# Kernel optimization log

Measured on AMD Instinct MI355X. Metric: run time of the kernel, lower is better.

## Reference

```python
import jax, jax.numpy as jnp
import numpy as np

S, B, D, H, V, TOK = 512, 32, 512, 512, 64, 30000
L = 2  # num LSTM layers


def _lstm_dir(x, Wih, Whh, bih, bhh, reverse):
    # x: [S, B, Din]; Wih: [4H, Din]; Whh: [4H, H]
    Bn = x.shape[1]
    Hn = Whh.shape[1]

    def step(carry, xt):
        h, c = carry
        g = xt @ Wih.T + h @ Whh.T + bih + bhh  # [B, 4H]
        i, f, gg, o = jnp.split(g, 4, axis=-1)  # torch gate order i,f,g,o
        c = jax.nn.sigmoid(f) * c + jax.nn.sigmoid(i) * jnp.tanh(gg)
        h = jax.nn.sigmoid(o) * jnp.tanh(c)
        return (h, c), h

    init = (jnp.zeros((Bn, Hn), x.dtype), jnp.zeros((Bn, Hn), x.dtype))
    _, hs = jax.lax.scan(step, init, x, reverse=reverse)
    return hs  # [S, B, H], time-aligned with x


def _bilstm(x, Wih0, Whh0, bih0, bhh0, Wih1, Whh1, bih1, bhh1):
    # layer 0
    hf = _lstm_dir(x, Wih0[0], Whh0[0], bih0[0], bhh0[0], reverse=False)
    hb = _lstm_dir(x, Wih0[1], Whh0[1], bih0[1], bhh0[1], reverse=True)
    x = jnp.concatenate([hf, hb], axis=-1)  # [S, B, 2H]
    # layer 1
    hf = _lstm_dir(x, Wih1[0], Whh1[0], bih1[0], bhh1[0], reverse=False)
    hb = _lstm_dir(x, Wih1[1], Whh1[1], bih1[1], bhh1[1], reverse=True)
    return jnp.concatenate([hf, hb], axis=-1)  # [S, B, 2H]


def setup_inputs() -> dict:
    key = jax.random.key(0)
    ks = jax.random.split(key, 16)
    s = 0.05
    inp = {}
    inp['source'] = jax.random.randint(ks[0], (S, B), 0, TOK)
    inp['target'] = jax.random.randint(ks[1], (S, B), 0, V)
    inp['emb'] = jax.random.normal(ks[2], (TOK, D), jnp.float32) * s
    inp['Wih0'] = jax.random.normal(ks[3], (2, 4 * H, D), jnp.float32) * s
    inp['Whh0'] = jax.random.normal(ks[4], (2, 4 * H, H), jnp.float32) * s
    inp['bih0'] = jax.random.normal(ks[5], (2, 4 * H), jnp.float32) * s
    inp['bhh0'] = jax.random.normal(ks[6], (2, 4 * H), jnp.float32) * s
    inp['Wih1'] = jax.random.normal(ks[7], (2, 4 * H, 2 * H), jnp.float32) * s
    inp['Whh1'] = jax.random.normal(ks[8], (2, 4 * H, H), jnp.float32) * s
    inp['bih1'] = jax.random.normal(ks[9], (2, 4 * H), jnp.float32) * s
    inp['bhh1'] = jax.random.normal(ks[10], (2, 4 * H), jnp.float32) * s
    inp['Wout'] = jax.random.normal(ks[11], (V, 2 * H), jnp.float32) * s
    inp['bout'] = jax.random.normal(ks[12], (V,), jnp.float32) * s
    inp['trans'] = jax.random.uniform(ks[13], (V, V), jnp.float32)  # torch.rand
    return inp


def reference(source, target, emb, Wih0, Whh0, bih0, bhh0, Wih1, Whh1, bih1, bhh1, Wout, bout, trans):
    # get_logits: frozen embedding -> BiLSTM -> linear
    x = jax.lax.stop_gradient(emb[source])  # [S, B, D] (embedding under no_grad)
    h = _bilstm(x, Wih0, Whh0, bih0, bhh0, Wih1, Whh1, bih1, bhh1)  # [S, B, 2H]
    logits = (h @ Wout.T + bout)[:, 0, :]  # [S, V] -- forward() decodes batch 0

    # Viterbi: max-plus recurrence over time
    def vstep(delta, lt):
        scores = delta[:, None] + trans + lt[None, :]  # [V_prev, V_cur]
        return jnp.max(scores, axis=0), jnp.argmax(scores, axis=0)

    delta, bps = jax.lax.scan(vstep, logits[0], logits[1:])  # bps: [S-1, V]
    last = jnp.argmax(delta)

    def back(idx, bp):
        prev = bp[idx]
        return prev, prev

    _, rev = jax.lax.scan(back, last, bps, reverse=True)  # rev[t] = tag at t, t in [0, S-2]
    path = jnp.concatenate([rev, last[None]]).astype(jnp.int32)  # [S]
    return path
```

## Files before the change

kernel.cpp:

```cpp
#include <hip/hip_runtime.h>
#include <stdint.h>

constexpr int kS = 512;
constexpr int kB = 32;
constexpr int kH = 512;
constexpr int kV = 64;


__device__ __forceinline__ float fast_sigmoid(float x) {
  return __builtin_amdgcn_rcpf(1.0f + __expf(-x));
}
__device__ __forceinline__ float fast_tanh(float x) {
  return 1.0f - 2.0f * __builtin_amdgcn_rcpf(1.0f + __expf(2.0f * x));
}
__device__ __forceinline__ float bcast(float v, int k) {
  return __uint_as_float(__builtin_amdgcn_readlane(__float_as_uint(v), k));
}
__device__ __forceinline__ unsigned ld_l2(const unsigned* p) {
  unsigned r;
  asm volatile("global_load_dword %0, %1, off sc0\n\ts_waitcnt vmcnt(0)"
               : "=v"(r) : "v"(p) : "memory");
  return r;
}
__device__ __forceinline__ void st_l2(unsigned* p, unsigned v) {
  asm volatile("global_store_dword %0, %1, off sc0" :: "v"(p), "v"(v)
               : "memory");
}

__global__ __launch_bounds__(128) void k_embed(const int* __restrict__ src,
                                               const float* __restrict__ emb,
                                               float* __restrict__ X) {
  const int t = blockIdx.x;
  const int s = src[t * kB];
  const float4* e = (const float4*)(emb + (size_t)s * 512);
  float4* x = (float4*)(X + (size_t)t * 512);
  x[threadIdx.x] = e[threadIdx.x];
}

template <int KZ>
__global__ __launch_bounds__(512, 1) void k_rec(
    const float* __restrict__ Z0,
    const float* __restrict__ Z1,
    const float* __restrict__ Wih,
    const float* __restrict__ Whh,
    const float* __restrict__ bih,
    const float* __restrict__ bhh,
    float* __restrict__ HL,
    float* __restrict__ HG) {
  constexpr int ZPW = KZ / 8;
  __shared__ float part[64 * 9];
  const int b = blockIdx.x;
  const int xslot = b & 7;
  if (xslot > 1) return;
  const int dir = xslot, wg = b >> 3;
  const int tid = threadIdx.x;
  const int wv = tid >> 6, l = tid & 63;
  const float* WihB = Wih + (size_t)dir * 2048 * KZ;
  const float* WhhB = Whh + (size_t)dir * 2048 * 512;
  float* HbL = HL + (size_t)dir * kS * kH;
  float* HbG = HG + (size_t)dir * kS * kH;
  const int grow = (l >> 4) * 512 + wg * 16 + (l & 15);

  float ww[64];
  {
    const float* wp = WhhB + (size_t)grow * 512 + wv * 64;
#pragma unroll
    for (int i = 0; i < 64; i += 4) {
      const float4 v = *(const float4*)(wp + i);
      ww[i] = v.x; ww[i + 1] = v.y; ww[i + 2] = v.z; ww[i + 3] = v.w;
    }
  }
  float zw[ZPW];
  {
    const float* zp = WihB + (size_t)grow * KZ + wv * ZPW;
#pragma unroll
    for (int i = 0; i < ZPW; i += 4) {
      const float4 v = *(const float4*)(zp + i);
      zw[i] = v.x; zw[i + 1] = v.y; zw[i + 2] = v.z; zw[i + 3] = v.w;
    }
  }
  float bias = 0.0f;
  if (wv == 0) bias = bih[dir * 2048 + grow] + bhh[dir * 2048 + grow];
  float cstate = 0.0f;

  const float* zbase = (KZ == 512) ? Z0 : ((wv < 4) ? Z0 : Z1);
  const int zoff = (KZ == 512) ? tid : ((wv & 3) * 128 + l);

  const int t0 = dir ? (kS - 1) : 0;
  float zc0 = zbase[(size_t)t0 * 512 + zoff];
  float zc1 = (KZ == 1024) ? zbase[(size_t)t0 * 512 + zoff + 64] : 0.0f;

  for (int s = 0; s < kS; s++) {
    const int t = dir ? (kS - 1 - s) : s;
    int tn = dir ? (t - 1) : (t + 1);
    if (tn < 0) tn = 0;
    if (tn > kS - 1) tn = kS - 1;
    const float zn0 = zbase[(size_t)tn * 512 + zoff];
    const float zn1 = (KZ == 1024) ? zbase[(size_t)tn * 512 + zoff + 64] : 0.0f;

    float a0 = 0.f, a1 = 0.f, a2 = 0.f, a3 = 0.f;
#pragma unroll
    for (int k = 0; k < 64; k += 4) {
      a0 += zw[k + 0] * bcast(zc0, k + 0);
      a1 += zw[k + 1] * bcast(zc0, k + 1);
      a2 += zw[k + 2] * bcast(zc0, k + 2);
      a3 += zw[k + 3] * bcast(zc0, k + 3);
    }
    if (KZ == 1024) {
#pragma unroll
      for (int k = 0; k < 64; k += 4) {
        a0 += zw[64 + k + 0] * bcast(zc1, k + 0);
        a1 += zw[64 + k + 1] * bcast(zc1, k + 1);
        a2 += zw[64 + k + 2] * bcast(zc1, k + 2);
        a3 += zw[64 + k + 3] * bcast(zc1, k + 3);
      }
    }

    float hreg = 0.0f;
    if (s > 0) {
      const int tp = dir ? (t + 1) : (t - 1);
      const unsigned* lp = (const unsigned*)(HbL + (size_t)tp * kH) + tid;
      const unsigned* gp = (const unsigned*)(HbG + (size_t)tp * kH) + tid;
      unsigned u = ld_l2(lp);
#pragma unroll 1
      for (int r = 0; r < 4; r++) {
        if (u != 0xFFFFFFFFu) break;
        u = ld_l2(lp);
      }
      while (u == 0xFFFFFFFFu)
        u = __hip_atomic_load(gp, __ATOMIC_RELAXED, __HIP_MEMORY_SCOPE_AGENT);
      hreg = __uint_as_float(u);
    }

#pragma unroll
    for (int k = 0; k < 64; k += 4) {
      a0 += ww[k + 0] * bcast(hreg, k + 0);
      a1 += ww[k + 1] * bcast(hreg, k + 1);
      a2 += ww[k + 2] * bcast(hreg, k + 2);
      a3 += ww[k + 3] * bcast(hreg, k + 3);
    }
    part[l * 9 + wv] = (a0 + a1) + (a2 + a3);
    __syncthreads();
    if (wv == 0) {
      float ssum = bias;
#pragma unroll
      for (int w = 0; w < 8; w++) ssum += part[l * 9 + w];
      const float sf = __shfl(ssum, (l + 16) & 63);
      const float sg = __shfl(ssum, (l + 32) & 63);
      const float so = __shfl(ssum, (l + 48) & 63);
      if (l < 16) {
        const float ig = fast_sigmoid(ssum);
        const float fg = fast_sigmoid(sf);
        const float og = fast_sigmoid(so);
        cstate = fg * cstate + ig * fast_tanh(sg);
        const float h = og * fast_tanh(cstate);
        const unsigned hv = __float_as_uint(h);
        unsigned* lq = (unsigned*)(HbL + (size_t)t * kH) + wg * 16 + l;
        unsigned* gq = (unsigned*)(HbG + (size_t)t * kH) + wg * 16 + l;
        st_l2(lq, hv);
        __hip_atomic_store(gq, hv, __ATOMIC_RELAXED,
                           __HIP_MEMORY_SCOPE_AGENT);
      }
    }
    zc0 = zn0;
    zc1 = zn1;
  }
}

__global__ __launch_bounds__(256) void k_logits(const float* __restrict__ H1,
                                                const float* __restrict__ Wout,
                                                const float* __restrict__ bout,
                                                float* __restrict__ LOG) {
  __shared__ float hl[1024];
  const int t = blockIdx.x;
  const int tid = threadIdx.x;
  float4* hl4 = (float4*)hl;
  if (tid < 128)
    hl4[tid] = ((const float4*)(H1 + (size_t)t * kH))[tid];
  else
    hl4[tid] = ((const float4*)(H1 + (size_t)(kS + t) * kH))[tid - 128];
  __syncthreads();
  const int v = tid >> 2, q = tid & 3;
  const float4* w4 = (const float4*)(Wout + (size_t)v * 1024);
  float4 a = {0, 0, 0, 0};
#pragma unroll 8
  for (int j = 0; j < 64; j++) {
    const int idx = j * 4 + q;
    const float4 w = w4[idx];
    const float4 x = hl4[idx];
    a.x += w.x * x.x; a.y += w.y * x.y; a.z += w.z * x.z; a.w += w.w * x.w;
  }
  float acc = (a.x + a.y) + (a.z + a.w);
  acc += __shfl_xor(acc, 1);
  acc += __shfl_xor(acc, 2);
  if (q == 0) LOG[(size_t)t * kV + v] = acc + bout[v];
}

__global__ __launch_bounds__(256) void k_viterbi(const float* __restrict__ LOG,
                                                 const float* __restrict__ trans,
                                                 int* __restrict__ out) {
  __shared__ float delta[64];
  __shared__ float redS[4 * 64];
  __shared__ int redA[4 * 64];
  __shared__ unsigned char bp[511 * 64];
  const int tid = threadIdx.x;
  const int c = tid & 63, q = tid >> 6;
  if (tid < 64) delta[tid] = LOG[tid];
  __syncthreads();
  for (int t = 1; t < kS; t++) {
    float best = -1e30f;
    int bi = 0;
#pragma unroll 4
    for (int pp = 0; pp < 16; pp++) {
      const int p = q * 16 + pp;
      const float sc = delta[p] + trans[p * 64 + c];
      if (sc > best) { best = sc; bi = p; }
    }
    redS[q * 64 + c] = best;
    redA[q * 64 + c] = bi;
    __syncthreads();
    if (tid < 64) {
      float b = redS[c];
      int a = redA[c];
      for (int qq = 1; qq < 4; qq++) {
        const float v2 = redS[qq * 64 + c];
        if (v2 > b) { b = v2; a = redA[qq * 64 + c]; }
      }
      bp[(t - 1) * 64 + c] = (unsigned char)a;
      delta[c] = b + LOG[t * 64 + c];
    }
    __syncthreads();
  }
  if (tid == 0) {
    float b = delta[0];
    int a = 0;
    for (int i = 1; i < 64; i++)
      if (delta[i] > b) { b = delta[i]; a = i; }
    int idx = a;
    out[kS - 1] = idx;
    for (int t = kS - 2; t >= 0; t--) {
      idx = bp[t * 64 + idx];
      out[t] = idx;
    }
  }
}

extern "C" void kernel_launch(void* const* d_in, const int* in_sizes, int n_in,
                              void* d_out, int out_size, void* d_ws,
                              size_t ws_size, hipStream_t stream) {
  (void)in_sizes; (void)n_in; (void)out_size; (void)ws_size;
  const int* source  = (const int*)d_in[0];
  const float* emb   = (const float*)d_in[2];
  const float* Wih0  = (const float*)d_in[3];
  const float* Whh0  = (const float*)d_in[4];
  const float* bih0  = (const float*)d_in[5];
  const float* bhh0  = (const float*)d_in[6];
  const float* Wih1  = (const float*)d_in[7];
  const float* Whh1  = (const float*)d_in[8];
  const float* bih1  = (const float*)d_in[9];
  const float* bhh1  = (const float*)d_in[10];
  const float* Wout  = (const float*)d_in[11];
  const float* bout  = (const float*)d_in[12];
  const float* trans = (const float*)d_in[13];

  float* ws = (float*)d_ws;
  float* X   = ws;
  float* H0L = ws + 262144;
  float* H0G = ws + 786432;
  float* H1L = ws + 1310720;
  float* H1G = ws + 1835008;
  float* LOG = ws + 2359296;

  hipMemsetAsync(H0L, 0xFF, (size_t)4 * 524288 * sizeof(float), stream);

  k_embed<<<kS, 128, 0, stream>>>(source, emb, X);
  k_rec<512><<<256, 512, 0, stream>>>(X, X, Wih0, Whh0, bih0, bhh0, H0L, H0G);
  k_rec<1024><<<256, 512, 0, stream>>>(H0G, H0G + 262144, Wih1, Whh1, bih1,
                                       bhh1, H1L, H1G);
  k_logits<<<kS, 256, 0, stream>>>(H1G, Wout, bout, LOG);
  k_viterbi<<<1, 256, 0, stream>>>(LOG, trans, (int*)d_out);
}
```

Before: 2.045 ms.

## Claim LSTM work slots by hardware XCC id and parallelize gate activations

```diff
diff --git a/kernel.cpp b/kernel.cpp
--- a/kernel.cpp
+++ b/kernel.cpp
@@ -46,14 +46,25 @@
     const float* __restrict__ bih,
     const float* __restrict__ bhh,
     float* __restrict__ HL,
-    float* __restrict__ HG) {
+    float* __restrict__ HG,
+    int* __restrict__ claims) {
   constexpr int ZPW = KZ / 8;
   __shared__ float part[64 * 9];
-  const int b = blockIdx.x;
-  const int xslot = b & 7;
-  if (xslot > 1) return;
-  const int dir = xslot, wg = b >> 3;
+  __shared__ int claim_s;
   const int tid = threadIdx.x;
+
+  if (tid == 0) {
+    unsigned x;
+    asm volatile("s_getreg_b32 %0, hwreg(HW_REG_XCC_ID)" : "=s"(x));
+    x &= 7u;
+    const int r = atomicAdd(claims + x, 1);
+    claim_s = (x < 2u && r < 32) ? (int)((x << 5) | r) : -1;
+  }
+  __syncthreads();
+  const int cl = claim_s;
+  if (cl < 0) return;
+  const int dir = cl >> 5, wg = cl & 31;
+
   const int wv = tid >> 6, l = tid & 63;
   const float* WihB = Wih + (size_t)dir * 2048 * KZ;
   const float* WhhB = Whh + (size_t)dir * 2048 * 512;
@@ -123,7 +134,7 @@
       const unsigned* gp = (const unsigned*)(HbG + (size_t)tp * kH) + tid;
       unsigned u = ld_l2(lp);
 #pragma unroll 1
-      for (int r = 0; r < 4; r++) {
+      for (int r = 0; r < 64; r++) {
         if (u != 0xFFFFFFFFu) break;
         u = ld_l2(lp);
       }
@@ -145,14 +156,13 @@
       float ssum = bias;
 #pragma unroll
       for (int w = 0; w < 8; w++) ssum += part[l * 9 + w];
-      const float sf = __shfl(ssum, (l + 16) & 63);
-      const float sg = __shfl(ssum, (l + 32) & 63);
-      const float so = __shfl(ssum, (l + 48) & 63);
+      const float act = (l >= 32 && l < 48) ? fast_tanh(ssum)
+                                            : fast_sigmoid(ssum);
+      const float fg = __shfl(act, (l + 16) & 63);
+      const float gt = __shfl(act, (l + 32) & 63);
+      const float og = __shfl(act, (l + 48) & 63);
       if (l < 16) {
-        const float ig = fast_sigmoid(ssum);
-        const float fg = fast_sigmoid(sf);
-        const float og = fast_sigmoid(so);
-        cstate = fg * cstate + ig * fast_tanh(sg);
+        cstate = fg * cstate + act * gt;
         const float h = og * fast_tanh(cstate);
         const unsigned hv = __float_as_uint(h);
         unsigned* lq = (unsigned*)(HbL + (size_t)t * kH) + wg * 16 + l;
@@ -270,13 +280,16 @@
   float* H1L = ws + 1310720;
   float* H1G = ws + 1835008;
   float* LOG = ws + 2359296;
+  int*   CLM = (int*)(ws + 2392064);
 
   hipMemsetAsync(H0L, 0xFF, (size_t)4 * 524288 * sizeof(float), stream);
+  hipMemsetAsync(CLM, 0, 16 * sizeof(int), stream);
 
   k_embed<<<kS, 128, 0, stream>>>(source, emb, X);
-  k_rec<512><<<256, 512, 0, stream>>>(X, X, Wih0, Whh0, bih0, bhh0, H0L, H0G);
+  k_rec<512><<<256, 512, 0, stream>>>(X, X, Wih0, Whh0, bih0, bhh0, H0L, H0G,
+                                      CLM);
   k_rec<1024><<<256, 512, 0, stream>>>(H0G, H0G + 262144, Wih1, Whh1, bih1,
-                                       bhh1, H1L, H1G);
+                                       bhh1, H1L, H1G, CLM + 8);
   k_logits<<<kS, 256, 0, stream>>>(H1G, Wout, bout, LOG);
   k_viterbi<<<1, 256, 0, stream>>>(LOG, trans, (int*)d_out);
 }
```

After: 6.427 ms. +214.3%, slower.
